# Kernel tuning notes

Measured on AMD Instinct MI355X. Metric: run time of the kernel, lower is better.

Reference implementation:

```python
import jax, jax.numpy as jnp
import numpy as np

M, K, E = 4096, 7168, 2048  # tokens, hidden_size, expert_dim

def setup_inputs() -> dict:
    key = jax.random.key(0)
    k1, k2, k3 = jax.random.split(key, 3)
    x = jax.random.normal(k1, (M, K), dtype=jnp.float32)
    # NT layout: weights stored [n, k]
    w_up_gate = jax.random.normal(k2, (2 * E, K), dtype=jnp.float32) * (1.0 / np.sqrt(K))
    w_down = jax.random.normal(k3, (K, E), dtype=jnp.float32) * (1.0 / np.sqrt(E))
    return {"x": x, "w_up_gate": w_up_gate, "w_down": w_down}

def reference(x, w_up_gate, w_down):
    # up_gate GEMM: [m, k] @ [n, k]^T -> [m, 2*E]
    ug = jnp.einsum('mk,nk->mn', x, w_up_gate)
    gate, up = jnp.split(ug, 2, axis=-1)          # each [m, E]
    h = jax.nn.silu(gate) * up                     # SwiGLU activation
    # down GEMM: [m, E] @ [hidden, E]^T -> [m, hidden]
    out = jnp.einsum('me,he->mh', h, w_down)
    return out
```

## Files before the change

### kernel.cpp

```cpp
#include <hip/hip_runtime.h>
#include <hip/hip_bf16.h>
#include <stdint.h>

typedef __attribute__((ext_vector_type(8))) short     bf16x8;
typedef __attribute__((ext_vector_type(4))) float     f32x4;

__device__ __forceinline__ unsigned short f2bf(float f) {
  unsigned int u = __float_as_uint(f);
  u += 0x7FFFu + ((u >> 16) & 1u);
  return (unsigned short)(u >> 16);
}

__device__ __forceinline__ void async_cp16(const void* g, void* l) {
  __builtin_amdgcn_global_load_lds((const __attribute__((address_space(1))) void*)g,
                                   (__attribute__((address_space(3))) void*)l,
                                   16, 0, 0);
}

__global__ __launch_bounds__(256) void cvt_all(const float* __restrict__ x,
                                               const float* __restrict__ wug,
                                               const float* __restrict__ wd,
                                               unsigned short* __restrict__ xb,
                                               unsigned short* __restrict__ wub,
                                               unsigned short* __restrict__ wdb) {
  int i = blockIdx.x * blockDim.x + threadIdx.x;
  const int stride = gridDim.x * blockDim.x;
  for (; i < 18350080; i += stride) {
    float4 v; ushort4* dp;
    if (i < 7340032) {
      v = ((const float4*)x)[i];
      dp = (ushort4*)xb + i;
    } else if (i < 14680064) {
      const int k = i - 7340032;
      const int r = k / 1792, c = k - r * 1792;
      const int g = r >> 5, w = r & 31;
      const int src = g * 16 + (w & 15) + ((w & 16) ? 2048 : 0);
      v = ((const float4*)wug)[(size_t)src * 1792 + c];
      dp = (ushort4*)wub + k;
    } else {
      const int k = i - 14680064;
      v = ((const float4*)wd)[k];
      dp = (ushort4*)wdb + k;
    }
    ushort4 o;
    o.x = f2bf(v.x); o.y = f2bf(v.y); o.z = f2bf(v.z); o.w = f2bf(v.w);
    *dp = o;
  }
}

template <int K, int N, bool FUSE_SWIGLU>
__global__ __launch_bounds__(512, 1) void gemm_nt(const unsigned short* __restrict__ A,
                                                  const unsigned short* __restrict__ B,
                                                  void* __restrict__ Cv) {
  extern __shared__ char sm[];
  constexpr int nbx = N / 256;
  constexpr int nwg = (4096 / 256) * nbx;
  constexpr size_t K2 = (size_t)K * 2;
  constexpr int nt = K / 64;

  const int bid = blockIdx.x;
  constexpr int q8 = nwg / 8;
  const int swz = (bid & 7) * q8 + (bid >> 3);
  const int bx = swz % nbx, by = swz / nbx;
  const int row0 = by * 256, col0 = bx * 256;

  const int tid = threadIdx.x, wave = tid >> 6, lane = tid & 63;
  const int wr = wave >> 2, wc = wave & 3;
  const int fr = lane & 15, fg = lane >> 4;

  const int l3 = lane >> 3, p7 = lane & 7;
  const int qgl = p7 ^ l3;
  const char* srcA = (const char*)A + (size_t)(row0 + wave * 8 + l3) * K2 + qgl * 16;
  const char* srcB = (const char*)B + (size_t)(col0 + wave * 8 + l3) * K2 + qgl * 16;
  const int dstq = wave * 1024 + lane * 16;

#define STAGE_AQ(qa, tt, bufo) \
  async_cp16(srcA + (size_t)(qa) * 64 * K2 + (size_t)(tt) * 128, \
             sm + (bufo) + (qa) * 8192 + dstq)
#define STAGE_BQ(qb, tt, bufo) \
  async_cp16(srcB + (size_t)(qb) * 64 * K2 + (size_t)(tt) * 128, \
             sm + (bufo) + 32768 + (qb) * 8192 + dstq)

  const int s0 = ((fg) ^ (fr & 7)) << 4;
  const int s1 = ((4 + fg) ^ (fr & 7)) << 4;
  const int offAb = wr * 16384 + fr * 128;
  const int offBb = 32768 + wc * 8192 + fr * 128;

  f32x4 acc[8][4];
#pragma unroll
  for (int m = 0; m < 8; ++m)
#pragma unroll
    for (int n = 0; n < 4; ++n) acc[m][n] = (f32x4){0.f, 0.f, 0.f, 0.f};

  STAGE_AQ(0, 0, 0); STAGE_AQ(2, 0, 0);
  STAGE_BQ(0, 0, 0); STAGE_BQ(1, 0, 0); STAGE_BQ(2, 0, 0); STAGE_BQ(3, 0, 0);
  STAGE_AQ(1, 0, 0); STAGE_AQ(3, 0, 0);
  asm volatile("s_waitcnt vmcnt(2)" ::: "memory");
  __builtin_amdgcn_s_barrier();

  for (int t = 0; t < nt; ++t) {
    const char* cur = sm + (t & 1) * 65536;
    const int nxo = ((t + 1) & 1) * 65536;
    const bool more = (t + 1 < nt);

    bf16x8 a0[4][2], b0[2][2], b1[2][2];
#pragma unroll
    for (int mt = 0; mt < 4; ++mt) {
      a0[mt][0] = *(const bf16x8*)(cur + offAb + mt * 2048 + s0);
      a0[mt][1] = *(const bf16x8*)(cur + offAb + mt * 2048 + s1);
    }
#pragma unroll
    for (int n = 0; n < 2; ++n) {
      b0[n][0] = *(const bf16x8*)(cur + offBb + n * 2048 + s0);
      b0[n][1] = *(const bf16x8*)(cur + offBb + n * 2048 + s1);
      b1[n][0] = *(const bf16x8*)(cur + offBb + (n + 2) * 2048 + s0);
      b1[n][1] = *(const bf16x8*)(cur + offBb + (n + 2) * 2048 + s1);
    }
    if (more) {
      STAGE_AQ(0, t + 1, nxo); STAGE_AQ(2, t + 1, nxo);
      STAGE_BQ(0, t + 1, nxo); STAGE_BQ(1, t + 1, nxo);
      STAGE_BQ(2, t + 1, nxo); STAGE_BQ(3, t + 1, nxo);
    }
    __builtin_amdgcn_s_setprio(1);
#pragma unroll
    for (int kk = 0; kk < 2; ++kk)
#pragma unroll
      for (int mt = 0; mt < 4; ++mt) {
#pragma unroll
        for (int n = 0; n < 2; ++n)
          acc[mt][n] = __builtin_amdgcn_mfma_f32_16x16x32_bf16(a0[mt][kk], b0[n][kk], acc[mt][n], 0, 0, 0);
#pragma unroll
        for (int n = 0; n < 2; ++n)
          acc[mt][n + 2] = __builtin_amdgcn_mfma_f32_16x16x32_bf16(a0[mt][kk], b1[n][kk], acc[mt][n + 2], 0, 0, 0);
      }
    __builtin_amdgcn_s_setprio(0);
    if (more) { asm volatile("s_waitcnt vmcnt(6)" ::: "memory"); }
    else      { asm volatile("s_waitcnt vmcnt(0)" ::: "memory"); }
    __builtin_amdgcn_s_barrier();

    bf16x8 a1[4][2];
#pragma unroll
    for (int mt = 0; mt < 4; ++mt) {
      a1[mt][0] = *(const bf16x8*)(cur + offAb + (mt + 4) * 2048 + s0);
      a1[mt][1] = *(const bf16x8*)(cur + offAb + (mt + 4) * 2048 + s1);
    }
    if (more) { STAGE_AQ(1, t + 1, nxo); STAGE_AQ(3, t + 1, nxo); }
    __builtin_amdgcn_s_setprio(1);
#pragma unroll
    for (int kk = 0; kk < 2; ++kk)
#pragma unroll
      for (int mt = 0; mt < 4; ++mt) {
#pragma unroll
        for (int n = 0; n < 2; ++n)
          acc[mt + 4][n + 2] = __builtin_amdgcn_mfma_f32_16x16x32_bf16(a1[mt][kk], b1[n][kk], acc[mt + 4][n + 2], 0, 0, 0);
#pragma unroll
        for (int n = 0; n < 2; ++n)
          acc[mt + 4][n] = __builtin_amdgcn_mfma_f32_16x16x32_bf16(a1[mt][kk], b0[n][kk], acc[mt + 4][n], 0, 0, 0);
      }
    __builtin_amdgcn_s_setprio(0);
    if (more) {
      asm volatile("s_waitcnt vmcnt(2)" ::: "memory");
      __builtin_amdgcn_s_barrier();
    }
  }
#undef STAGE_AQ
#undef STAGE_BQ

  const int rowb = row0 + wr * 128 + fg * 4;
  if (FUSE_SWIGLU) {
    unsigned short* Hp = (unsigned short*)Cv;
    const int ecb = ((col0 + wc * 64) >> 1) + fr;
#pragma unroll
    for (int m = 0; m < 8; ++m)
#pragma unroll
      for (int p = 0; p < 2; ++p)
#pragma unroll
        for (int j = 0; j < 4; ++j) {
          const float gv = acc[m][2 * p][j];
          const float uv = acc[m][2 * p + 1][j];
          const float s  = gv / (1.0f + __expf(-gv));
          Hp[(size_t)(rowb + m * 16 + j) * (N / 2) + (ecb + p * 16)] = f2bf(s * uv);
        }
  } else {
    float* Cp = (float*)Cv;
    const int colb = col0 + wc * 64 + fr;
#pragma unroll
    for (int m = 0; m < 8; ++m)
#pragma unroll
      for (int n = 0; n < 4; ++n)
#pragma unroll
        for (int j = 0; j < 4; ++j)
          Cp[(size_t)(rowb + m * 16 + j) * N + (colb + n * 16)] = acc[m][n][j];
  }
}

extern "C" void kernel_launch(void* const* d_in, const int* in_sizes, int n_in,
                              void* d_out, int out_size, void* d_ws, size_t ws_size,
                              hipStream_t stream) {
  const int M = 4096, K = 7168, E = 2048;

  const float* x   = (const float*)d_in[0];
  const float* wug = (const float*)d_in[1];
  const float* wd  = (const float*)d_in[2];
  float* out = (float*)d_out;

  char* ws = (char*)d_ws;
  unsigned short* xb  = (unsigned short*)(ws);
  unsigned short* wub = (unsigned short*)(ws + 58720256);
  unsigned short* wdb = (unsigned short*)(ws + 117440512);
  unsigned short* h   = (unsigned short*)(ws + 146800640);
  if (ws_size < 163577856) return;

  hipFuncSetAttribute((const void*)gemm_nt<7168, 4096, true>,
                      hipFuncAttributeMaxDynamicSharedMemorySize, 131072);
  hipFuncSetAttribute((const void*)gemm_nt<2048, 7168, false>,
                      hipFuncAttributeMaxDynamicSharedMemorySize, 131072);

  cvt_all<<<2048, 256, 0, stream>>>(x, wug, wd, xb, wub, wdb);

  gemm_nt<7168, 4096, true><<<256, 512, 131072, stream>>>(xb, wub, h);

  gemm_nt<2048, 7168, false><<<448, 512, 131072, stream>>>(h, wdb, out);
}
```

Baseline: 376.2 us.

## Switch GEMM inner loop to 32x32x16 bf16 MFMA with matching layouts

Replaces the 16x16x32 MFMA tiling with 32x32x16 MFMA instructions, reorganizing the per-wave accumulators into 4x2 tiles of 32x32. The LDS read pattern, swizzle offsets, epilogue row mapping and the gate/up interleave in the weight conversion (now 32-row groups) are all updated to match. Larger MFMA tiles halve the LDS fragment loads per FLOP and issue fewer instructions, at the cost of different register pressure and epilogue store patterns.

```diff
diff --git a/kernel.cpp b/kernel.cpp
--- a/kernel.cpp
+++ b/kernel.cpp
@@ -2,8 +2,8 @@
 #include <hip/hip_bf16.h>
 #include <stdint.h>
 
-typedef __attribute__((ext_vector_type(8))) short     bf16x8;
-typedef __attribute__((ext_vector_type(4))) float     f32x4;
+typedef __attribute__((ext_vector_type(8)))  short bf16x8;
+typedef __attribute__((ext_vector_type(16))) float f32x16;
 
 __device__ __forceinline__ unsigned short f2bf(float f) {
   unsigned int u = __float_as_uint(f);
@@ -33,8 +33,8 @@
     } else if (i < 14680064) {
       const int k = i - 7340032;
       const int r = k / 1792, c = k - r * 1792;
-      const int g = r >> 5, w = r & 31;
-      const int src = g * 16 + (w & 15) + ((w & 16) ? 2048 : 0);
+      const int g = r >> 6, w = r & 63;
+      const int src = g * 32 + (w & 31) + ((w & 32) ? 2048 : 0);
       v = ((const float4*)wug)[(size_t)src * 1792 + c];
       dp = (ushort4*)wub + k;
     } else {
@@ -66,7 +66,7 @@
 
   const int tid = threadIdx.x, wave = tid >> 6, lane = tid & 63;
   const int wr = wave >> 2, wc = wave & 3;
-  const int fr = lane & 15, fg = lane >> 4;
+  const int l31 = lane & 31, hi = lane >> 5;
 
   const int l3 = lane >> 3, p7 = lane & 7;
   const int qgl = p7 ^ l3;
@@ -81,16 +81,23 @@
   async_cp16(srcB + (size_t)(qb) * 64 * K2 + (size_t)(tt) * 128, \
              sm + (bufo) + 32768 + (qb) * 8192 + dstq)
 
-  const int s0 = ((fg) ^ (fr & 7)) << 4;
-  const int s1 = ((4 + fg) ^ (fr & 7)) << 4;
-  const int offAb = wr * 16384 + fr * 128;
-  const int offBb = 32768 + wc * 8192 + fr * 128;
-
-  f32x4 acc[8][4];
-#pragma unroll
-  for (int m = 0; m < 8; ++m)
-#pragma unroll
-    for (int n = 0; n < 4; ++n) acc[m][n] = (f32x4){0.f, 0.f, 0.f, 0.f};
+  const int r7 = l31 & 7;
+  int sA[4], sB[4];
+#pragma unroll
+  for (int kst = 0; kst < 4; ++kst) {
+    sA[kst] = (((kst << 1) | hi) ^ r7) << 4;
+    sB[kst] = sA[kst];
+  }
+  const int offAb = wr * 128 * 128 + l31 * 128;
+  const int offBb = 32768 + wc * 64 * 128 + l31 * 128;
+
+  f32x16 acc[4][2];
+#pragma unroll
+  for (int m = 0; m < 4; ++m)
+#pragma unroll
+    for (int n = 0; n < 2; ++n)
+#pragma unroll
+      for (int j = 0; j < 16; ++j) acc[m][n][j] = 0.f;
 
   STAGE_AQ(0, 0, 0); STAGE_AQ(2, 0, 0);
   STAGE_BQ(0, 0, 0); STAGE_BQ(1, 0, 0); STAGE_BQ(2, 0, 0); STAGE_BQ(3, 0, 0);
@@ -103,19 +110,17 @@
     const int nxo = ((t + 1) & 1) * 65536;
     const bool more = (t + 1 < nt);
 
-    bf16x8 a0[4][2], b0[2][2], b1[2][2];
-#pragma unroll
-    for (int mt = 0; mt < 4; ++mt) {
-      a0[mt][0] = *(const bf16x8*)(cur + offAb + mt * 2048 + s0);
-      a0[mt][1] = *(const bf16x8*)(cur + offAb + mt * 2048 + s1);
-    }
-#pragma unroll
-    for (int n = 0; n < 2; ++n) {
-      b0[n][0] = *(const bf16x8*)(cur + offBb + n * 2048 + s0);
-      b0[n][1] = *(const bf16x8*)(cur + offBb + n * 2048 + s1);
-      b1[n][0] = *(const bf16x8*)(cur + offBb + (n + 2) * 2048 + s0);
-      b1[n][1] = *(const bf16x8*)(cur + offBb + (n + 2) * 2048 + s1);
-    }
+    bf16x8 a0[2][4], b[2][4];
+#pragma unroll
+    for (int mt = 0; mt < 2; ++mt)
+#pragma unroll
+      for (int kst = 0; kst < 4; ++kst)
+        a0[mt][kst] = *(const bf16x8*)(cur + offAb + mt * 4096 + sA[kst]);
+#pragma unroll
+    for (int n = 0; n < 2; ++n)
+#pragma unroll
+      for (int kst = 0; kst < 4; ++kst)
+        b[n][kst] = *(const bf16x8*)(cur + offBb + n * 4096 + sB[kst]);
     if (more) {
       STAGE_AQ(0, t + 1, nxo); STAGE_AQ(2, t + 1, nxo);
       STAGE_BQ(0, t + 1, nxo); STAGE_BQ(1, t + 1, nxo);
@@ -123,40 +128,32 @@
     }
     __builtin_amdgcn_s_setprio(1);
 #pragma unroll
-    for (int kk = 0; kk < 2; ++kk)
-#pragma unroll
-      for (int mt = 0; mt < 4; ++mt) {
+    for (int kst = 0; kst < 4; ++kst)
+#pragma unroll
+      for (int mt = 0; mt < 2; ++mt)
 #pragma unroll
         for (int n = 0; n < 2; ++n)
-          acc[mt][n] = __builtin_amdgcn_mfma_f32_16x16x32_bf16(a0[mt][kk], b0[n][kk], acc[mt][n], 0, 0, 0);
-#pragma unroll
-        for (int n = 0; n < 2; ++n)
-          acc[mt][n + 2] = __builtin_amdgcn_mfma_f32_16x16x32_bf16(a0[mt][kk], b1[n][kk], acc[mt][n + 2], 0, 0, 0);
-      }
+          acc[mt][n] = __builtin_amdgcn_mfma_f32_32x32x16_bf16(a0[mt][kst], b[n][kst], acc[mt][n], 0, 0, 0);
     __builtin_amdgcn_s_setprio(0);
     if (more) { asm volatile("s_waitcnt vmcnt(6)" ::: "memory"); }
     else      { asm volatile("s_waitcnt vmcnt(0)" ::: "memory"); }
     __builtin_amdgcn_s_barrier();
 
-    bf16x8 a1[4][2];
-#pragma unroll
-    for (int mt = 0; mt < 4; ++mt) {
-      a1[mt][0] = *(const bf16x8*)(cur + offAb + (mt + 4) * 2048 + s0);
-      a1[mt][1] = *(const bf16x8*)(cur + offAb + (mt + 4) * 2048 + s1);
-    }
+    bf16x8 a1[2][4];
+#pragma unroll
+    for (int mt = 0; mt < 2; ++mt)
+#pragma unroll
+      for (int kst = 0; kst < 4; ++kst)
+        a1[mt][kst] = *(const bf16x8*)(cur + offAb + (mt + 2) * 4096 + sA[kst]);
     if (more) { STAGE_AQ(1, t + 1, nxo); STAGE_AQ(3, t + 1, nxo); }
     __builtin_amdgcn_s_setprio(1);
 #pragma unroll
-    for (int kk = 0; kk < 2; ++kk)
-#pragma unroll
-      for (int mt = 0; mt < 4; ++mt) {
+    for (int kst = 0; kst < 4; ++kst)
+#pragma unroll
+      for (int mt = 0; mt < 2; ++mt)
 #pragma unroll
         for (int n = 0; n < 2; ++n)
-          acc[mt + 4][n + 2] = __builtin_amdgcn_mfma_f32_16x16x32_bf16(a1[mt][kk], b1[n][kk], acc[mt + 4][n + 2], 0, 0, 0);
-#pragma unroll
-        for (int n = 0; n < 2; ++n)
-          acc[mt + 4][n] = __builtin_amdgcn_mfma_f32_16x16x32_bf16(a1[mt][kk], b0[n][kk], acc[mt + 4][n], 0, 0, 0);
-      }
+          acc[mt + 2][n] = __builtin_amdgcn_mfma_f32_32x32x16_bf16(a1[mt][kst], b[n][kst], acc[mt + 2][n], 0, 0, 0);
     __builtin_amdgcn_s_setprio(0);
     if (more) {
       asm volatile("s_waitcnt vmcnt(2)" ::: "memory");
@@ -166,31 +163,32 @@
 #undef STAGE_AQ
 #undef STAGE_BQ
 
-  const int rowb = row0 + wr * 128 + fg * 4;
+  const int rowb = row0 + wr * 128;
   if (FUSE_SWIGLU) {
     unsigned short* Hp = (unsigned short*)Cv;
-    const int ecb = ((col0 + wc * 64) >> 1) + fr;
-#pragma unroll
-    for (int m = 0; m < 8; ++m)
-#pragma unroll
-      for (int p = 0; p < 2; ++p)
-#pragma unroll
-        for (int j = 0; j < 4; ++j) {
-          const float gv = acc[m][2 * p][j];
-          const float uv = acc[m][2 * p + 1][j];
-          const float s  = gv / (1.0f + __expf(-gv));
-          Hp[(size_t)(rowb + m * 16 + j) * (N / 2) + (ecb + p * 16)] = f2bf(s * uv);
-        }
+    const int ecb = ((col0 + wc * 64) >> 1) + l31;
+#pragma unroll
+    for (int mt = 0; mt < 4; ++mt)
+#pragma unroll
+      for (int j = 0; j < 16; ++j) {
+        const int row = rowb + mt * 32 + (j & 3) + 8 * (j >> 2) + 4 * hi;
+        const float gv = acc[mt][0][j];
+        const float uv = acc[mt][1][j];
+        const float s  = gv / (1.0f + __expf(-gv));
+        Hp[(size_t)row * (N / 2) + ecb] = f2bf(s * uv);
+      }
   } else {
     float* Cp = (float*)Cv;
-    const int colb = col0 + wc * 64 + fr;
-#pragma unroll
-    for (int m = 0; m < 8; ++m)
-#pragma unroll
-      for (int n = 0; n < 4; ++n)
-#pragma unroll
-        for (int j = 0; j < 4; ++j)
-          Cp[(size_t)(rowb + m * 16 + j) * N + (colb + n * 16)] = acc[m][n][j];
+    const int colb = col0 + wc * 64 + l31;
+#pragma unroll
+    for (int mt = 0; mt < 4; ++mt)
+#pragma unroll
+      for (int n = 0; n < 2; ++n)
+#pragma unroll
+        for (int j = 0; j < 16; ++j) {
+          const int row = rowb + mt * 32 + (j & 3) + 8 * (j >> 2) + 4 * hi;
+          Cp[(size_t)row * N + (colb + n * 32)] = acc[mt][n][j];
+        }
   }
 }
 
```

After: 415.1 us. 10.3% more time.
